# Kernel optimization log

Measured on AMD Instinct MI355X. Metric: run time of the kernel, lower is better.

## Reference

```python
import jax, jax.numpy as jnp
import numpy as np
import math

PHI = (1 + math.sqrt(5)) / 2
TABLE_SIZE = 4096
TWO_PI = 2.0 * math.pi
_ang = np.arange(TABLE_SIZE, dtype=np.float32) * (TWO_PI / TABLE_SIZE)
SIN_T = jnp.asarray(np.sin(_ang))
COS_T = jnp.asarray(np.cos(_ang))


def lookup_sin_cos(theta):
    """LUT sin/cos with linear interpolation over a 4096-entry table on [0, 2pi)."""
    pos = (theta / TWO_PI % 1.0) * TABLE_SIZE
    i0f = jnp.floor(pos)
    frac = pos - i0f
    i0 = i0f.astype(jnp.int32) % TABLE_SIZE
    i1 = (i0 + 1) % TABLE_SIZE
    s = SIN_T[i0] * (1.0 - frac) + SIN_T[i1] * frac
    c = COS_T[i0] * (1.0 - frac) + COS_T[i1] * frac
    return s, c


def setup_inputs() -> dict:
    key = jax.random.key(0)
    ks = jax.random.split(key, 8)
    B, S, D, H = 2, 2048, 1024, 16
    dh = D // H
    return {
        "x": jax.random.normal(ks[0], (B, S, D), dtype=jnp.float32),
        "w_q": jax.random.normal(ks[1], (H, dh), dtype=jnp.float32) * 0.02,
        "b_q": jnp.zeros((H, dh), jnp.float32),
        "phi_q": jnp.full((H, dh), PHI, jnp.float32),
        "w_k": jax.random.normal(ks[2], (H, dh), dtype=jnp.float32) * 0.02,
        "b_k": jnp.zeros((H, dh), jnp.float32),
        "phi_k": jnp.full((H, dh), PHI, jnp.float32),
        "w_v": jax.random.normal(ks[3], (H, dh), dtype=jnp.float32) * 0.02,
        "b_v": jnp.zeros((H, dh), jnp.float32),
        "w_out": jax.random.normal(ks[4], (D,), dtype=jnp.float32) * 0.02,
        "b_out": jnp.zeros((D,), jnp.float32),
    }


def reference(x, w_q, b_q, phi_q, w_k, b_k, phi_k, w_v, b_v, w_out, b_out):
    B, S, D = x.shape
    H, dh = w_q.shape
    scale = math.sqrt(2 * dh)
    t = jnp.arange(S, dtype=x.dtype).reshape(1, S, 1, 1)
    xh = x.reshape(B, S, H, dh)

    theta_q = xh / (1.0 + jnp.abs(w_q)) + b_q + t * phi_q
    sin_q, cos_q = lookup_sin_cos(theta_q)
    Q = jnp.concatenate([cos_q, sin_q], axis=-1)  # (B,S,H,2dh)

    theta_k = xh / (1.0 + jnp.abs(w_k)) + b_k + t * phi_k
    sin_k, cos_k = lookup_sin_cos(theta_k)
    K = jnp.concatenate([cos_k, sin_k], axis=-1)  # (B,S,H,2dh)

    theta_v = xh / (1.0 + jnp.abs(w_v)) + b_v
    sin_v, cos_v = lookup_sin_cos(theta_v)
    V = cos_v + sin_v  # (B,S,H,dh)

    scores = jnp.einsum('bqhd,bkhd->bhqk', Q, K) / scale
    causal = jnp.triu(jnp.ones((S, S), dtype=bool), k=1)
    scores = jnp.where(causal, -jnp.inf, scores)
    attn = jax.nn.softmax(scores, axis=-1)
    out = jnp.einsum('bhqk,bkhd->bqhd', attn, V).reshape(B, S, D)

    theta_out = out / (1.0 + jnp.abs(w_out)) + b_out
    sin_o, cos_o = lookup_sin_cos(theta_out)
    return cos_o + sin_o
```

## Files before the change

### kernel.cpp

```cpp
#include <hip/hip_runtime.h>
#include <hip/hip_bf16.h>
#include <math.h>

#define BB 2
#define SS 2048
#define HH 16
#define DH 64
#define DQK 128
#define DD (HH*DH)
#define QS2   0.12751758f
#define EBIAS 11.5415605f

typedef _Float16 half8_t __attribute__((ext_vector_type(8)));
typedef _Float16 half4_t __attribute__((ext_vector_type(4)));
typedef float f32x4_t __attribute__((ext_vector_type(4)));
typedef float f32x4v __attribute__((ext_vector_type(4)));

__device__ __forceinline__ void fsincos(float th, float* sn, float* cs) {
  float rev = th * 0.15915494309189535f;
  rev -= floorf(rev);
  float ang = rev * 6.283185307179586f;
  *sn = __sinf(ang);
  *cs = __cosf(ang);
}

__device__ __forceinline__ void dma16(const void* g, void* l) {
  __builtin_amdgcn_global_load_lds(
      (const __attribute__((address_space(1))) unsigned int*)g,
      (__attribute__((address_space(3))) unsigned int*)l, 16, 0, 0);
}

__global__ __launch_bounds__(256) void gen_qkv(
    const float* __restrict__ x,
    const float* __restrict__ wq, const float* __restrict__ bq,
    const float* __restrict__ phq,
    const float* __restrict__ wk, const float* __restrict__ bk,
    const float* __restrict__ phk,
    const float* __restrict__ wv, const float* __restrict__ bv,
    _Float16* __restrict__ Qd, _Float16* __restrict__ Kd, _Float16* __restrict__ Vtd)
{
  int stile = blockIdx.x & 31;
  int bh    = blockIdx.x >> 5;
  int b = bh >> 4, h = bh & 15;
  int t = threadIdx.x;
  int sl = t >> 2;
  int dq = (t & 3) << 4;
  int s  = stile * 64 + sl;

  __shared__ _Float16 Vl[64 * 65];

  const float* xr = x + (((size_t)b * SS + s) * HH + h) * DH + dq;
  float xv[16];
#pragma unroll
  for (int i = 0; i < 4; i++)
    *(f32x4v*)(&xv[i * 4]) = *(const f32x4v*)(xr + i * 4);

  float tv = (float)s;
  _Float16 qc[16], qs[16], kc[16], ks[16];
#pragma unroll
  for (int i = 0; i < 16; i++) {
    int d = dq + i;
    int hd = h * DH + d;
    {
      float th = xv[i] / (1.f + fabsf(wq[hd])) + bq[hd] + tv * phq[hd];
      float sn, cs; fsincos(th, &sn, &cs);
      qc[i] = (_Float16)(cs * QS2);
      qs[i] = (_Float16)(sn * QS2);
    }
    {
      float th = xv[i] / (1.f + fabsf(wk[hd])) + bk[hd] + tv * phk[hd];
      float sn, cs; fsincos(th, &sn, &cs);
      kc[i] = (_Float16)cs;
      ks[i] = (_Float16)sn;
    }
    {
      float th = xv[i] / (1.f + fabsf(wv[hd])) + bv[hd];
      float sn, cs; fsincos(th, &sn, &cs);
      Vl[d * 65 + sl] = (_Float16)(cs + sn);
    }
  }
  size_t qbase = ((size_t)bh * SS + s) * DQK;
#pragma unroll
  for (int i = 0; i < 2; i++) {
    *(half8_t*)(Qd + qbase + dq + i * 8)      = *(half8_t*)(&qc[i * 8]);
    *(half8_t*)(Qd + qbase + DH + dq + i * 8) = *(half8_t*)(&qs[i * 8]);
  }
  {
    size_t ktb = ((size_t)bh * 32 + stile) * 8192;
    int fo0 = (t & 3) * 2;
    *(half8_t*)(Kd + ktb + ((size_t)(fo0    ) * 64 + sl) * 8) = *(half8_t*)(&kc[0]);
    *(half8_t*)(Kd + ktb + ((size_t)(fo0 + 1) * 64 + sl) * 8) = *(half8_t*)(&kc[8]);
    *(half8_t*)(Kd + ktb + ((size_t)(fo0 + 8) * 64 + sl) * 8) = *(half8_t*)(&ks[0]);
    *(half8_t*)(Kd + ktb + ((size_t)(fo0 + 9) * 64 + sl) * 8) = *(half8_t*)(&ks[8]);
  }
  __syncthreads();
#pragma unroll
  for (int i = 0; i < 2; i++) {
    int u = t * 2 + i;
    int dv = u & 63, ku = u >> 6;
    _Float16 tmp[8];
#pragma unroll
    for (int jj = 0; jj < 8; jj++) tmp[jj] = Vl[dv * 65 + ku * 8 + jj];
    *(half8_t*)(Vtd + (((size_t)bh * 32 + stile) * 8 + ku) * 512 + dv * 8) =
        *(half8_t*)tmp;
  }
}

__global__ __launch_bounds__(256) void flash_attn(
    const _Float16* __restrict__ Qd, const _Float16* __restrict__ Kd,
    const _Float16* __restrict__ Vtd,
    const float* __restrict__ wout, const float* __restrict__ bout,
    float* __restrict__ out)
{
  int qt = 31 - (blockIdx.x >> 5);
  int bh = blockIdx.x & 31;
  int b  = bh >> 4, hh = bh & 15;
  int nch = qt + 1;
  int q0 = qt * 64;
  int wave = threadIdx.x >> 6;
  int lane = threadIdx.x & 63;
  int lm = lane & 15, lq = lane >> 4;
  int qh = wave >> 1;
  int kh = wave & 1;

  __shared__ __align__(16) _Float16 KV[2][12288];

  const _Float16* Kg = Kd + (size_t)bh * 32 * 8192;
  const _Float16* Vg = Vtd + (size_t)bh * 32 * 4096;

  {
#pragma unroll
    for (int i = 0; i < 4; i++)
      dma16(Kg + (size_t)(wave * 4 + i) * 512 + lane * 8, &KV[0][(wave * 4 + i) * 512]);
#pragma unroll
    for (int i = 0; i < 2; i++)
      dma16(Vg + (size_t)(wave * 2 + i) * 512 + lane * 8, &KV[0][8192 + (wave * 2 + i) * 512]);
  }

  const _Float16* Qb = Qd + ((size_t)bh * SS + q0 + qh * 32) * DQK;
  half8_t aq[2][4];
#pragma unroll
  for (int qtl = 0; qtl < 2; qtl++)
#pragma unroll
    for (int c = 0; c < 4; c++)
      aq[qtl][c] = *(const half8_t*)(Qb + (qtl * 16 + lm) * DQK + c * 32 + lq * 8);

  f32x4_t o[4][2];
  float l[2] = {0.f, 0.f};
#pragma unroll
  for (int dt = 0; dt < 4; dt++)
#pragma unroll
    for (int qtl = 0; qtl < 2; qtl++) o[dt][qtl] = (f32x4_t){0.f, 0.f, 0.f, 0.f};

  const f32x4_t cinit = (f32x4_t){-EBIAS, -EBIAS, -EBIAS, -EBIAS};

  for (int kt = 0; kt < nch; ++kt) {
    int bf = kt & 1;
    __syncthreads();
    if (kt + 1 < nch) {
      int nb = (kt + 1) & 1;
      const _Float16* gK = Kg + (size_t)(kt + 1) * 8192;
      const _Float16* gV = Vg + (size_t)(kt + 1) * 4096;
#pragma unroll
      for (int i = 0; i < 4; i++)
        dma16(gK + (size_t)(wave * 4 + i) * 512 + lane * 8, &KV[nb][(wave * 4 + i) * 512]);
#pragma unroll
      for (int i = 0; i < 2; i++)
        dma16(gV + (size_t)(wave * 2 + i) * 512 + lane * 8, &KV[nb][8192 + (wave * 2 + i) * 512]);
    }

    const _Float16* lK = &KV[bf][0];
    const _Float16* lV = &KV[bf][8192];
    int k0 = kt * 64;

    f32x4_t cST[2][2];
    cST[0][0] = cST[0][1] = cST[1][0] = cST[1][1] = cinit;
#pragma unroll
    for (int c = 0; c < 4; c++) {
      half8_t k0f = *(const half8_t*)(lK + ((size_t)(c * 4 + lq) * 64 + kh * 32 + lm) * 8);
      half8_t k1f = *(const half8_t*)(lK + ((size_t)(c * 4 + lq) * 64 + kh * 32 + 16 + lm) * 8);
      cST[0][0] = __builtin_amdgcn_mfma_f32_16x16x32_f16(k0f, aq[0][c], cST[0][0], 0, 0, 0);
      cST[0][1] = __builtin_amdgcn_mfma_f32_16x16x32_f16(k0f, aq[1][c], cST[0][1], 0, 0, 0);
      cST[1][0] = __builtin_amdgcn_mfma_f32_16x16x32_f16(k1f, aq[0][c], cST[1][0], 0, 0, 0);
      cST[1][1] = __builtin_amdgcn_mfma_f32_16x16x32_f16(k1f, aq[1][c], cST[1][1], 0, 0, 0);
    }

    bool maskit = (kt == nch - 1);
    half4_t pb[2][2];
#pragma unroll
    for (int ktl = 0; ktl < 2; ktl++)
#pragma unroll
      for (int qtl = 0; qtl < 2; qtl++) {
        float pf[4];
#pragma unroll
        for (int r = 0; r < 4; r++) {
          float sv = cST[ktl][qtl][r];
          if (maskit) {
            int key  = k0 + kh * 32 + ktl * 16 + lq * 4 + r;
            int qrow = q0 + qh * 32 + qtl * 16 + lm;
            if (key > qrow) sv = -1e30f;
          }
          pf[r] = __builtin_exp2f(sv);
          l[qtl] += pf[r];
        }
        pb[ktl][qtl] = (half4_t){(_Float16)pf[0], (_Float16)pf[1],
                                 (_Float16)pf[2], (_Float16)pf[3]};
      }

#pragma unroll
    for (int dt = 0; dt < 4; dt++)
#pragma unroll
      for (int kg = 0; kg < 2; kg++) {
        half4_t vf = *(const half4_t*)(lV +
            ((size_t)(kh * 4 + kg * 2 + (lq >> 1)) * 64 + dt * 16 + lm) * 8 + (lq & 1) * 4);
        o[dt][0] = __builtin_amdgcn_mfma_f32_16x16x16f16(vf, pb[kg][0], o[dt][0], 0, 0, 0);
        o[dt][1] = __builtin_amdgcn_mfma_f32_16x16x16f16(vf, pb[kg][1], o[dt][1], 0, 0, 0);
      }
  }

#pragma unroll
  for (int qtl = 0; qtl < 2; qtl++) {
    l[qtl] += __shfl_xor(l[qtl], 16);
    l[qtl] += __shfl_xor(l[qtl], 32);
  }

  int sc = nch & 1;
  float* Of = (float*)&KV[sc][0];
  float* Lf = Of + 64 * 68;
  __syncthreads();
  if (kh == 1) {
#pragma unroll
    for (int qtl = 0; qtl < 2; qtl++) {
      int row = qh * 32 + qtl * 16 + lm;
#pragma unroll
      for (int dt = 0; dt < 4; dt++)
#pragma unroll
        for (int r = 0; r < 4; r++)
          Of[row * 68 + dt * 16 + lq * 4 + r] = o[dt][qtl][r];
      if (lq == 0) Lf[row] = l[qtl];
    }
  }
  __syncthreads();
  if (kh == 0) {
#pragma unroll
    for (int qtl = 0; qtl < 2; qtl++) {
      int row = qh * 32 + qtl * 16 + lm;
      float rl = 1.f / (l[qtl] + Lf[row]);
#pragma unroll
      for (int dt = 0; dt < 4; dt++)
#pragma unroll
        for (int r = 0; r < 4; r++) {
          int idx = row * 68 + dt * 16 + lq * 4 + r;
          Of[idx] = (o[dt][qtl][r] + Of[idx]) * rl;
        }
    }
  }
  __syncthreads();
  {
    int dcol = hh * DH + lane;
    float iw = 1.f / (1.f + fabsf(wout[dcol]));
    float bo = bout[dcol];
#pragma unroll
    for (int rr = 0; rr < 16; rr++) {
      int row = wave * 16 + rr;
      float th = Of[row * 68 + lane] * iw + bo;
      float sn, cs; fsincos(th, &sn, &cs);
      out[((size_t)b * SS + q0 + row) * DD + dcol] = cs + sn;
    }
  }
}

extern "C" void kernel_launch(void* const* d_in, const int* in_sizes, int n_in,
                              void* d_out, int out_size, void* d_ws, size_t ws_size,
                              hipStream_t stream) {
  (void)in_sizes; (void)n_in; (void)out_size; (void)ws_size;
  const float* x   = (const float*)d_in[0];
  const float* wq  = (const float*)d_in[1];
  const float* bq  = (const float*)d_in[2];
  const float* phq = (const float*)d_in[3];
  const float* wk  = (const float*)d_in[4];
  const float* bk  = (const float*)d_in[5];
  const float* phk = (const float*)d_in[6];
  const float* wv  = (const float*)d_in[7];
  const float* bv  = (const float*)d_in[8];
  const float* wo  = (const float*)d_in[9];
  const float* bo  = (const float*)d_in[10];

  _Float16* Qd  = (_Float16*)d_ws;
  _Float16* Kd  = Qd + (size_t)BB * HH * SS * DQK;
  _Float16* Vtd = Kd + (size_t)BB * HH * SS * DQK;

  gen_qkv<<<BB * HH * (SS / 64), 256, 0, stream>>>(
      x, wq, bq, phq, wk, bk, phk, wv, bv, Qd, Kd, Vtd);
  flash_attn<<<32 * 32, 256, 0, stream>>>(
      Qd, Kd, Vtd, wo, bo, (float*)d_out);
}
```

Measured before the change: 141.3 us.

## Load V straight to registers, use native sin/cos and rcp, vectorize params

In the attention kernel, V tiles are now read from global memory directly into registers each iteration instead of being staged in LDS by asynchronous copies. This shrinks the shared buffer to K only and frees LDS for more resident blocks, but V load latency is exposed inside the loop. The QKV generator now loads its parameters as float4 vectors and swaps the block-index mapping. Throughout, sin/cos use the hardware builtins that take the angle in revolutions, and divisions become approximate reciprocals, trading a little accuracy for fewer instructions.

```diff
diff --git a/kernel.cpp b/kernel.cpp
--- a/kernel.cpp
+++ b/kernel.cpp
@@ -19,9 +19,22 @@
 __device__ __forceinline__ void fsincos(float th, float* sn, float* cs) {
   float rev = th * 0.15915494309189535f;
   rev -= floorf(rev);
+#if __has_builtin(__builtin_amdgcn_sinf) && __has_builtin(__builtin_amdgcn_cosf)
+  *sn = __builtin_amdgcn_sinf(rev);
+  *cs = __builtin_amdgcn_cosf(rev);
+#else
   float ang = rev * 6.283185307179586f;
   *sn = __sinf(ang);
   *cs = __cosf(ang);
+#endif
+}
+
+__device__ __forceinline__ float frcp(float v) {
+#if __has_builtin(__builtin_amdgcn_rcpf)
+  return __builtin_amdgcn_rcpf(v);
+#else
+  return 1.f / v;
+#endif
 }
 
 __device__ __forceinline__ void dma16(const void* g, void* l) {
@@ -39,8 +52,8 @@
     const float* __restrict__ wv, const float* __restrict__ bv,
     _Float16* __restrict__ Qd, _Float16* __restrict__ Kd, _Float16* __restrict__ Vtd)
 {
-  int stile = blockIdx.x & 31;
-  int bh    = blockIdx.x >> 5;
+  int stile = blockIdx.x >> 5;
+  int bh    = blockIdx.x & 31;
   int b = bh >> 4, h = bh & 15;
   int t = threadIdx.x;
   int sl = t >> 2;
@@ -50,33 +63,41 @@
   __shared__ _Float16 Vl[64 * 65];
 
   const float* xr = x + (((size_t)b * SS + s) * HH + h) * DH + dq;
-  float xv[16];
-#pragma unroll
-  for (int i = 0; i < 4; i++)
-    *(f32x4v*)(&xv[i * 4]) = *(const f32x4v*)(xr + i * 4);
-
   float tv = (float)s;
+  int hd0 = h * DH + dq;
   _Float16 qc[16], qs[16], kc[16], ks[16];
 #pragma unroll
-  for (int i = 0; i < 16; i++) {
-    int d = dq + i;
-    int hd = h * DH + d;
-    {
-      float th = xv[i] / (1.f + fabsf(wq[hd])) + bq[hd] + tv * phq[hd];
-      float sn, cs; fsincos(th, &sn, &cs);
-      qc[i] = (_Float16)(cs * QS2);
-      qs[i] = (_Float16)(sn * QS2);
-    }
-    {
-      float th = xv[i] / (1.f + fabsf(wk[hd])) + bk[hd] + tv * phk[hd];
-      float sn, cs; fsincos(th, &sn, &cs);
-      kc[i] = (_Float16)cs;
-      ks[i] = (_Float16)sn;
-    }
-    {
-      float th = xv[i] / (1.f + fabsf(wv[hd])) + bv[hd];
-      float sn, cs; fsincos(th, &sn, &cs);
-      Vl[d * 65 + sl] = (_Float16)(cs + sn);
+  for (int g = 0; g < 4; g++) {
+    f32x4v x4  = *(const f32x4v*)(xr + g * 4);
+    f32x4v wq4 = *(const f32x4v*)(wq + hd0 + g * 4);
+    f32x4v bq4 = *(const f32x4v*)(bq + hd0 + g * 4);
+    f32x4v pq4 = *(const f32x4v*)(phq + hd0 + g * 4);
+    f32x4v wk4 = *(const f32x4v*)(wk + hd0 + g * 4);
+    f32x4v bk4 = *(const f32x4v*)(bk + hd0 + g * 4);
+    f32x4v pk4 = *(const f32x4v*)(phk + hd0 + g * 4);
+    f32x4v wv4 = *(const f32x4v*)(wv + hd0 + g * 4);
+    f32x4v bv4 = *(const f32x4v*)(bv + hd0 + g * 4);
+#pragma unroll
+    for (int i2 = 0; i2 < 4; i2++) {
+      int i = g * 4 + i2;
+      float xv = x4[i2];
+      {
+        float th = xv * frcp(1.f + fabsf(wq4[i2])) + fmaf(tv, pq4[i2], bq4[i2]);
+        float sn, cs; fsincos(th, &sn, &cs);
+        qc[i] = (_Float16)(cs * QS2);
+        qs[i] = (_Float16)(sn * QS2);
+      }
+      {
+        float th = xv * frcp(1.f + fabsf(wk4[i2])) + fmaf(tv, pk4[i2], bk4[i2]);
+        float sn, cs; fsincos(th, &sn, &cs);
+        kc[i] = (_Float16)cs;
+        ks[i] = (_Float16)sn;
+      }
+      {
+        float th = xv * frcp(1.f + fabsf(wv4[i2])) + bv4[i2];
+        float sn, cs; fsincos(th, &sn, &cs);
+        Vl[(dq + i) * 65 + sl] = (_Float16)(cs + sn);
+      }
     }
   }
   size_t qbase = ((size_t)bh * SS + s) * DQK;
@@ -123,7 +144,7 @@
   int qh = wave >> 1;
   int kh = wave & 1;
 
-  __shared__ __align__(16) _Float16 KV[2][12288];
+  __shared__ __align__(16) _Float16 KB[2][8192];
 
   const _Float16* Kg = Kd + (size_t)bh * 32 * 8192;
   const _Float16* Vg = Vtd + (size_t)bh * 32 * 4096;
@@ -131,10 +152,7 @@
   {
 #pragma unroll
     for (int i = 0; i < 4; i++)
-      dma16(Kg + (size_t)(wave * 4 + i) * 512 + lane * 8, &KV[0][(wave * 4 + i) * 512]);
-#pragma unroll
-    for (int i = 0; i < 2; i++)
-      dma16(Vg + (size_t)(wave * 2 + i) * 512 + lane * 8, &KV[0][8192 + (wave * 2 + i) * 512]);
+      dma16(Kg + (size_t)(wave * 4 + i) * 512 + lane * 8, &KB[0][(wave * 4 + i) * 512]);
   }
 
   const _Float16* Qb = Qd + ((size_t)bh * SS + q0 + qh * 32) * DQK;
@@ -153,24 +171,33 @@
     for (int qtl = 0; qtl < 2; qtl++) o[dt][qtl] = (f32x4_t){0.f, 0.f, 0.f, 0.f};
 
   const f32x4_t cinit = (f32x4_t){-EBIAS, -EBIAS, -EBIAS, -EBIAS};
+
+  const _Float16* Vw = Vg + ((size_t)(lq >> 1) * 64 + lm) * 8 + (lq & 1) * 4 +
+                       (size_t)kh * 4 * 64 * 8;
 
   for (int kt = 0; kt < nch; ++kt) {
     int bf = kt & 1;
     __syncthreads();
+
+    half4_t vr[4][2];
+    {
+      const _Float16* vsrc = Vw + (size_t)kt * 4096;
+#pragma unroll
+      for (int dt = 0; dt < 4; dt++)
+#pragma unroll
+        for (int kg = 0; kg < 2; kg++)
+          vr[dt][kg] = *(const half4_t*)(vsrc + ((size_t)kg * 2 * 64 + dt * 16) * 8);
+    }
+
     if (kt + 1 < nch) {
       int nb = (kt + 1) & 1;
       const _Float16* gK = Kg + (size_t)(kt + 1) * 8192;
-      const _Float16* gV = Vg + (size_t)(kt + 1) * 4096;
 #pragma unroll
       for (int i = 0; i < 4; i++)
-        dma16(gK + (size_t)(wave * 4 + i) * 512 + lane * 8, &KV[nb][(wave * 4 + i) * 512]);
-#pragma unroll
-      for (int i = 0; i < 2; i++)
-        dma16(gV + (size_t)(wave * 2 + i) * 512 + lane * 8, &KV[nb][8192 + (wave * 2 + i) * 512]);
-    }
-
-    const _Float16* lK = &KV[bf][0];
-    const _Float16* lV = &KV[bf][8192];
+        dma16(gK + (size_t)(wave * 4 + i) * 512 + lane * 8, &KB[nb][(wave * 4 + i) * 512]);
+    }
+
+    const _Float16* lK = &KB[bf][0];
     int k0 = kt * 64;
 
     f32x4_t cST[2][2];
@@ -211,10 +238,8 @@
     for (int dt = 0; dt < 4; dt++)
 #pragma unroll
       for (int kg = 0; kg < 2; kg++) {
-        half4_t vf = *(const half4_t*)(lV +
-            ((size_t)(kh * 4 + kg * 2 + (lq >> 1)) * 64 + dt * 16 + lm) * 8 + (lq & 1) * 4);
-        o[dt][0] = __builtin_amdgcn_mfma_f32_16x16x16f16(vf, pb[kg][0], o[dt][0], 0, 0, 0);
-        o[dt][1] = __builtin_amdgcn_mfma_f32_16x16x16f16(vf, pb[kg][1], o[dt][1], 0, 0, 0);
+        o[dt][0] = __builtin_amdgcn_mfma_f32_16x16x16f16(vr[dt][kg], pb[kg][0], o[dt][0], 0, 0, 0);
+        o[dt][1] = __builtin_amdgcn_mfma_f32_16x16x16f16(vr[dt][kg], pb[kg][1], o[dt][1], 0, 0, 0);
       }
   }
 
@@ -224,8 +249,7 @@
     l[qtl] += __shfl_xor(l[qtl], 32);
   }
 
-  int sc = nch & 1;
-  float* Of = (float*)&KV[sc][0];
+  float* Of = (float*)&KB[0][0];
   float* Lf = Of + 64 * 68;
   __syncthreads();
   if (kh == 1) {
@@ -245,7 +269,7 @@
 #pragma unroll
     for (int qtl = 0; qtl < 2; qtl++) {
       int row = qh * 32 + qtl * 16 + lm;
-      float rl = 1.f / (l[qtl] + Lf[row]);
+      float rl = frcp(l[qtl] + Lf[row]);
 #pragma unroll
       for (int dt = 0; dt < 4; dt++)
 #pragma unroll
@@ -258,7 +282,7 @@
   __syncthreads();
   {
     int dcol = hh * DH + lane;
-    float iw = 1.f / (1.f + fabsf(wout[dcol]));
+    float iw = frcp(1.f + fabsf(wout[dcol]));
     float bo = bout[dcol];
 #pragma unroll
     for (int rr = 0; rr < 16; rr++) {
```

Result: no change. 141.6 us (+0.2%).
